# Kernel tuning notes

Hardware: AMD Instinct MI355X
Metric: run time of the kernel (lower is better)

## Reference

```python
import jax, jax.numpy as jnp
import numpy as np


def setup_inputs() -> dict:
    key = jax.random.key(0)
    k1, k2, k3 = jax.random.split(key, 3)
    B, H, S, D = 2, 16, 2048, 64
    return {
        "q": jax.random.normal(k1, (B, H, S, D), dtype=jnp.float32),
        "k": jax.random.normal(k2, (B, H, S, D), dtype=jnp.float32),
        "v": jax.random.normal(k3, (B, H, S, D), dtype=jnp.float32),
        "chunk_size": 256,
    }


def reference(q, k, v, chunk_size):
    # Chunked Based linear attention: linear (K^T V) + rank-3 quadratic (K x K x V)
    # inter-chunk state recurrence (shifted/exclusive cumsum over chunks) plus the
    # intra-chunk causal part with kernel  s = q.k;  phi = s + 0.5*s^2.
    B, H, S, D = q.shape
    C = chunk_size
    N = S // C
    scale = D ** (-0.5)

    qc = (q * scale).reshape(B, H, N, C, D)
    kc = k.reshape(B, H, N, C, D)
    vc = v.reshape(B, H, N, C, D)

    # ---- linear inter-chunk state: shifted cumsum of K^T V per chunk ----
    KV = jnp.einsum("bhncd,bhnce->bhnde", kc, vc)            # (B,H,N,D,D)
    S_lin = jnp.cumsum(KV, axis=2) - KV                       # exclusive cumsum
    o_lin = jnp.einsum("bhncd,bhnde->bhnce", qc, S_lin)

    # ---- quadratic inter-chunk state: shifted cumsum of sum_c K_d K_e V_f ----
    KKV = jnp.einsum("bhncd,bhnce,bhncf->bhndef", kc, kc, vc)  # (B,H,N,D,D,D)
    S_quad = jnp.cumsum(KKV, axis=2) - KKV                     # exclusive cumsum
    o_quad = 0.5 * jnp.einsum("bhndef,bhncd,bhnce->bhncf", S_quad, qc, qc)

    # ---- intra-chunk causal quadratic attention ----
    A = jnp.einsum("bhncd,bhnmd->bhncm", qc, kc)               # (B,H,N,C,C)
    mask = jnp.tril(jnp.ones((C, C), dtype=bool))
    Ak = jnp.where(mask, A + 0.5 * A * A, 0.0)
    o_intra = jnp.einsum("bhncm,bhnmf->bhncf", Ak, vc)

    out = (o_lin + o_quad + o_intra).reshape(B, H, S, D)
    return out
```

## Files before the change

kernel.cpp:

```cpp
#include <hip/hip_runtime.h>
#include <stdint.h>

#define SEQ  2048
#define DH   64
#define BH_N 32
#define SCALE 0.125f

typedef __attribute__((ext_vector_type(8))) short short8;
typedef __attribute__((ext_vector_type(4))) short short4b;
typedef __attribute__((ext_vector_type(4))) float f32x4;

static __device__ __forceinline__ unsigned short f2bf(float f) {
  unsigned int u = __float_as_uint(f);
  u += 0x7fffu + ((u >> 16) & 1u);
  return (unsigned short)(u >> 16);
}
#if __has_builtin(__builtin_amdgcn_cvt_pk_bf16_f32)
typedef __attribute__((ext_vector_type(2))) __bf16 bf16x2;
static __device__ __forceinline__ unsigned packbf(float a, float b) {
  return __builtin_bit_cast(unsigned, __builtin_amdgcn_cvt_pk_bf16_f32(a, b));
}
#else
static __device__ __forceinline__ unsigned packbf(float a, float b) {
  unsigned ua = __float_as_uint(a); ua += 0x7fffu + ((ua >> 16) & 1u);
  unsigned ub = __float_as_uint(b); ub += 0x7fffu + ((ub >> 16) & 1u);
  return __builtin_amdgcn_perm(ub, ua, 0x07060302);
}
#endif

__global__ __launch_bounds__(256) void prep_kernel(
    const float* __restrict__ kin, const float* __restrict__ vin,
    unsigned short* __restrict__ kb2, unsigned short* __restrict__ vt2)
{
  const int sb = blockIdx.x;
  const int bh = blockIdx.y;
  const int t  = threadIdx.x;
  __shared__ __align__(16) unsigned short lds[4096];
  const size_t base  = ((size_t)bh * SEQ + (size_t)sb * 64) * DH;
  const size_t obase = ((size_t)bh * 32 + sb) * 4096;

  #pragma unroll
  for (int i = 0; i < 4; ++i) {
    int idx = i * 256 + t, key = idx >> 4, F = (idx & 15) * 4;
    float4 f = *reinterpret_cast<const float4*>(kin + base + key * DH + F);
    int c = (F >> 5) * 4 + ((F >> 3) & 3), jh = (F >> 2) & 1;
    uint2 pk; pk.x = packbf(f.x, f.y); pk.y = packbf(f.z, f.w);
    *reinterpret_cast<uint2*>(lds + (c * 64 + key) * 8 + jh * 4) = pk;
  }
  __syncthreads();
  #pragma unroll
  for (int uu = 0; uu < 2; ++uu) {
    int u = uu * 256 + t;
    *reinterpret_cast<uint4*>(kb2 + obase + u * 8) =
        *reinterpret_cast<const uint4*>(lds + u * 8);
  }
  __syncthreads();
  #pragma unroll
  for (int i = 0; i < 4; ++i) {
    int idx = i * 256 + t, key = idx >> 4, F = (idx & 15) * 4;
    float4 f = *reinterpret_cast<const float4*>(vin + base + key * DH + F);
    int kgp = key >> 5, qd = (key >> 2) & 3, jj = ((key >> 4) & 1) * 4 + (key & 3);
    int u0 = kgp * 256 + (F >> 4) * 64 + qd * 16 + (F & 15);
    lds[(u0 + 0) * 8 + jj] = f2bf(f.x);
    lds[(u0 + 1) * 8 + jj] = f2bf(f.y);
    lds[(u0 + 2) * 8 + jj] = f2bf(f.z);
    lds[(u0 + 3) * 8 + jj] = f2bf(f.w);
  }
  __syncthreads();
  #pragma unroll
  for (int uu = 0; uu < 2; ++uu) {
    int u = uu * 256 + t;
    *reinterpret_cast<uint4*>(vt2 + obase + u * 8) =
        *reinterpret_cast<const uint4*>(lds + u * 8);
  }
}

__global__ __launch_bounds__(256, 2) void attn_kernel(
    const float* __restrict__ q,
    const unsigned short* __restrict__ kb2,
    const unsigned short* __restrict__ vt2,
    float* __restrict__ out)
{
  const int b0   = blockIdx.x;
  const int bh   = b0 & 31;
  const int g    = b0 >> 5;
  const int j    = (g < 8) ? g : 23 - g;
  const int last = 2 * j + 1;
  const int tid  = threadIdx.x;
  const int w    = tid >> 6;
  const int lane = tid & 63;
  const int low  = lane & 15;
  const int quad = lane >> 4;
  const int rh   = w & 1;

  const int mytile = (w < 2) ? (2 * j + 1) : (2 * j);
  const int r0     = mytile * 64 + rh * 32;

  __shared__ __align__(16) unsigned short buf[2][8192];

  const unsigned short* kb_h = kb2 + (size_t)bh * 32 * 4096;
  const unsigned short* v2_h = vt2 + (size_t)bh * 32 * 4096;

  short8 aq[2][2];
  #pragma unroll
  for (int h = 0; h < 2; ++h) {
    const float* qp =
        q + ((size_t)bh * SEQ + r0 + h * 16 + low) * DH + quad * 8;
    #pragma unroll
    for (int ks = 0; ks < 2; ++ks) {
      float4 f0 = *reinterpret_cast<const float4*>(qp + ks * 32);
      float4 f1 = *reinterpret_cast<const float4*>(qp + ks * 32 + 4);
      uint4 uv;
      uv.x = packbf(f0.x * SCALE, f0.y * SCALE);
      uv.y = packbf(f0.z * SCALE, f0.w * SCALE);
      uv.z = packbf(f1.x * SCALE, f1.y * SCALE);
      uv.w = packbf(f1.z * SCALE, f1.w * SCALE);
      aq[h][ks] = __builtin_bit_cast(short8, uv);
    }
  }

  f32x4 oacc[2][4];
  #pragma unroll
  for (int h = 0; h < 2; ++h)
    #pragma unroll
    for (int i = 0; i < 4; ++i) oacc[h][i] = (f32x4){0.f, 0.f, 0.f, 0.f};

  const unsigned short* gsrc = (w < 2) ? kb_h : v2_h;
  const int ghalf  = (w & 1) * 2048;
  const int ldsoff = (w >> 1) * 4096 + ghalf;
  uint4 g0, g1, g2, g3;

  #define GLOAD(T)                                                             \
    do {                                                                       \
      const unsigned short* gs_ = gsrc + (size_t)(T) * 4096 + ghalf;           \
      g0 = *reinterpret_cast<const uint4*>(gs_ + 0 * 512 + lane * 8);          \
      g1 = *reinterpret_cast<const uint4*>(gs_ + 1 * 512 + lane * 8);          \
      g2 = *reinterpret_cast<const uint4*>(gs_ + 2 * 512 + lane * 8);          \
      g3 = *reinterpret_cast<const uint4*>(gs_ + 3 * 512 + lane * 8);          \
    } while (0)

  #define DSWRITE(B)                                                           \
    do {                                                                       \
      unsigned short* ld_ = &buf[B][ldsoff] + lane * 8;                        \
      *reinterpret_cast<uint4*>(ld_ + 0 * 512) = g0;                           \
      *reinterpret_cast<uint4*>(ld_ + 1 * 512) = g1;                           \
      *reinterpret_cast<uint4*>(ld_ + 2 * 512) = g2;                           \
      *reinterpret_cast<uint4*>(ld_ + 3 * 512) = g3;                           \
    } while (0)

  GLOAD(0);
  DSWRITE(0);

  for (int t = 0; t <= last; ++t) {
    const int bb = t & 1;
    if (t < last) GLOAD(t + 1);
    asm volatile("s_waitcnt lgkmcnt(0)" ::: "memory");
    __builtin_amdgcn_s_barrier();
    asm volatile("" ::: "memory");

    if (t <= mytile) {
      const bool diag = (t == mytile);
      const unsigned short* kT = &buf[bb][0];
      const unsigned short* vT = &buf[bb][4096];

      #pragma unroll
      for (int ntp = 0; ntp < 2; ++ntp) {
        short8 vf[4];
        #pragma unroll
        for (int ft = 0; ft < 4; ++ft)
          vf[ft] = *reinterpret_cast<const short8*>(
              vT + ((ntp * 4 + ft) * 64 + quad * 16 + low) * 8);

        #pragma unroll
        for (int sub = 0; sub < 2; ++sub) {
          const int nt = ntp * 2 + sub;
          f32x4 s0 = (f32x4){0.f, 0.f, 0.f, 0.f};
          f32x4 s1 = (f32x4){0.f, 0.f, 0.f, 0.f};
          #pragma unroll
          for (int ks = 0; ks < 2; ++ks) {
            short8 kf = *reinterpret_cast<const short8*>(
                kT + ((ks * 4 + quad) * 64 + nt * 16 + low) * 8);
            s0 = __builtin_amdgcn_mfma_f32_16x16x32_bf16(kf, aq[0][ks], s0, 0, 0, 0);
            s1 = __builtin_amdgcn_mfma_f32_16x16x32_bf16(kf, aq[1][ks], s1, 0, 0, 0);
          }
          #pragma unroll
          for (int h = 0; h < 2; ++h) {
            f32x4 sv = h ? s1 : s0;
            float pv[4];
            #pragma unroll
            for (int r = 0; r < 4; ++r) {
              float x = sv[r];
              pv[r] = __builtin_fmaf(0.5f * x, x, x);
            }
            if (diag) {
              #pragma unroll
              for (int r = 0; r < 4; ++r)
                if ((nt * 16 + quad * 4 + r) > (rh * 32 + h * 16 + low)) pv[r] = 0.f;
            }
            uint2 du; du.x = packbf(pv[0], pv[1]); du.y = packbf(pv[2], pv[3]);
            short4b pf = __builtin_bit_cast(short4b, du);
            #pragma unroll
            for (int ft = 0; ft < 4; ++ft) {
              short4b va = sub
                  ? __builtin_shufflevector(vf[ft], vf[ft], 4, 5, 6, 7)
                  : __builtin_shufflevector(vf[ft], vf[ft], 0, 1, 2, 3);
              oacc[h][ft] = __builtin_amdgcn_mfma_f32_16x16x16bf16_1k(
                  va, pf, oacc[h][ft], 0, 0, 0);
            }
          }
        }
      }
    }

    if (t < last) DSWRITE(bb ^ 1);
  }

  #pragma unroll
  for (int h = 0; h < 2; ++h)
    #pragma unroll
    for (int ft = 0; ft < 4; ++ft)
      *reinterpret_cast<f32x4*>(
          out + ((size_t)bh * SEQ + r0 + h * 16 + low) * DH + ft * 16 + quad * 4) =
          oacc[h][ft];
}

extern "C" void kernel_launch(void* const* d_in, const int* in_sizes, int n_in,
                              void* d_out, int out_size, void* d_ws, size_t ws_size,
                              hipStream_t stream)
{
  const float* q = (const float*)d_in[0];
  const float* k = (const float*)d_in[1];
  const float* v = (const float*)d_in[2];
  float* out = (float*)d_out;

  unsigned short* kb2 = (unsigned short*)d_ws;
  unsigned short* vt2 = kb2 + (size_t)BH_N * SEQ * DH;

  prep_kernel<<<dim3(32, BH_N), 256, 0, stream>>>(k, v, kb2, vt2);
  attn_kernel<<<512, 256, 0, stream>>>(q, kb2, vt2, out);
}
```

Measured before the change: 129.5 us.

## Use two waves per block, each owning a full 64-row query tile

Cuts the attention block from four waves to two. Each wave now handles 64 query rows (four 16-row groups) instead of 32, so every K fragment read from LDS feeds four MFMAs instead of two. Each wave also loads a whole 4096-element K or V tile into eight registers before staging it in LDS. This reduces LDS traffic per MFMA but doubles the accumulator and Q registers per wave and halves the waves per block, which may hurt latency hiding.

```diff
diff --git a/kernel.cpp b/kernel.cpp
--- a/kernel.cpp
+++ b/kernel.cpp
@@ -16,7 +16,6 @@
   return (unsigned short)(u >> 16);
 }
 #if __has_builtin(__builtin_amdgcn_cvt_pk_bf16_f32)
-typedef __attribute__((ext_vector_type(2))) __bf16 bf16x2;
 static __device__ __forceinline__ unsigned packbf(float a, float b) {
   return __builtin_bit_cast(unsigned, __builtin_amdgcn_cvt_pk_bf16_f32(a, b));
 }
@@ -75,7 +74,7 @@
   }
 }
 
-__global__ __launch_bounds__(256, 2) void attn_kernel(
+__global__ __launch_bounds__(128) void attn_kernel(
     const float* __restrict__ q,
     const unsigned short* __restrict__ kb2,
     const unsigned short* __restrict__ vt2,
@@ -86,24 +85,22 @@
   const int g    = b0 >> 5;
   const int j    = (g < 8) ? g : 23 - g;
   const int last = 2 * j + 1;
-  const int tid  = threadIdx.x;
-  const int w    = tid >> 6;
-  const int lane = tid & 63;
+  const int w    = threadIdx.x >> 6;
+  const int lane = threadIdx.x & 63;
   const int low  = lane & 15;
   const int quad = lane >> 4;
-  const int rh   = w & 1;
-
-  const int mytile = (w < 2) ? (2 * j + 1) : (2 * j);
-  const int r0     = mytile * 64 + rh * 32;
+
+  const int mytile = w ? (2 * j) : (2 * j + 1);
+  const int r0     = mytile * 64;
 
   __shared__ __align__(16) unsigned short buf[2][8192];
 
   const unsigned short* kb_h = kb2 + (size_t)bh * 32 * 4096;
   const unsigned short* v2_h = vt2 + (size_t)bh * 32 * 4096;
 
-  short8 aq[2][2];
-  #pragma unroll
-  for (int h = 0; h < 2; ++h) {
+  short8 aq[4][2];
+  #pragma unroll
+  for (int h = 0; h < 4; ++h) {
     const float* qp =
         q + ((size_t)bh * SEQ + r0 + h * 16 + low) * DH + quad * 8;
     #pragma unroll
@@ -119,33 +116,29 @@
     }
   }
 
-  f32x4 oacc[2][4];
-  #pragma unroll
-  for (int h = 0; h < 2; ++h)
+  f32x4 oacc[4][4];
+  #pragma unroll
+  for (int h = 0; h < 4; ++h)
     #pragma unroll
     for (int i = 0; i < 4; ++i) oacc[h][i] = (f32x4){0.f, 0.f, 0.f, 0.f};
 
-  const unsigned short* gsrc = (w < 2) ? kb_h : v2_h;
-  const int ghalf  = (w & 1) * 2048;
-  const int ldsoff = (w >> 1) * 4096 + ghalf;
-  uint4 g0, g1, g2, g3;
+  const unsigned short* gsrc = w ? v2_h : kb_h;
+  uint4 gr[8];
 
   #define GLOAD(T)                                                             \
     do {                                                                       \
-      const unsigned short* gs_ = gsrc + (size_t)(T) * 4096 + ghalf;           \
-      g0 = *reinterpret_cast<const uint4*>(gs_ + 0 * 512 + lane * 8);          \
-      g1 = *reinterpret_cast<const uint4*>(gs_ + 1 * 512 + lane * 8);          \
-      g2 = *reinterpret_cast<const uint4*>(gs_ + 2 * 512 + lane * 8);          \
-      g3 = *reinterpret_cast<const uint4*>(gs_ + 3 * 512 + lane * 8);          \
+      const unsigned short* gs_ = gsrc + (size_t)(T) * 4096;                   \
+      _Pragma("unroll")                                                        \
+      for (int r_ = 0; r_ < 8; ++r_)                                           \
+        gr[r_] = *reinterpret_cast<const uint4*>(gs_ + r_ * 512 + lane * 8);   \
     } while (0)
 
   #define DSWRITE(B)                                                           \
     do {                                                                       \
-      unsigned short* ld_ = &buf[B][ldsoff] + lane * 8;                        \
-      *reinterpret_cast<uint4*>(ld_ + 0 * 512) = g0;                           \
-      *reinterpret_cast<uint4*>(ld_ + 1 * 512) = g1;                           \
-      *reinterpret_cast<uint4*>(ld_ + 2 * 512) = g2;                           \
-      *reinterpret_cast<uint4*>(ld_ + 3 * 512) = g3;                           \
+      unsigned short* ld_ = &buf[B][w * 4096] + lane * 8;                      \
+      _Pragma("unroll")                                                        \
+      for (int r_ = 0; r_ < 8; ++r_)                                           \
+        *reinterpret_cast<uint4*>(ld_ + r_ * 512) = gr[r_];                    \
     } while (0)
 
   GLOAD(0);
@@ -174,28 +167,34 @@
         #pragma unroll
         for (int sub = 0; sub < 2; ++sub) {
           const int nt = ntp * 2 + sub;
-          f32x4 s0 = (f32x4){0.f, 0.f, 0.f, 0.f};
-          f32x4 s1 = (f32x4){0.f, 0.f, 0.f, 0.f};
-          #pragma unroll
-          for (int ks = 0; ks < 2; ++ks) {
-            short8 kf = *reinterpret_cast<const short8*>(
+          short8 kf[2];
+          #pragma unroll
+          for (int ks = 0; ks < 2; ++ks)
+            kf[ks] = *reinterpret_cast<const short8*>(
                 kT + ((ks * 4 + quad) * 64 + nt * 16 + low) * 8);
-            s0 = __builtin_amdgcn_mfma_f32_16x16x32_bf16(kf, aq[0][ks], s0, 0, 0, 0);
-            s1 = __builtin_amdgcn_mfma_f32_16x16x32_bf16(kf, aq[1][ks], s1, 0, 0, 0);
-          }
-          #pragma unroll
-          for (int h = 0; h < 2; ++h) {
-            f32x4 sv = h ? s1 : s0;
+
+          f32x4 s[4];
+          #pragma unroll
+          for (int h = 0; h < 4; ++h) s[h] = (f32x4){0.f, 0.f, 0.f, 0.f};
+          #pragma unroll
+          for (int ks = 0; ks < 2; ++ks)
+            #pragma unroll
+            for (int h = 0; h < 4; ++h)
+              s[h] = __builtin_amdgcn_mfma_f32_16x16x32_bf16(
+                  kf[ks], aq[h][ks], s[h], 0, 0, 0);
+
+          #pragma unroll
+          for (int h = 0; h < 4; ++h) {
             float pv[4];
             #pragma unroll
             for (int r = 0; r < 4; ++r) {
-              float x = sv[r];
+              float x = s[h][r];
               pv[r] = __builtin_fmaf(0.5f * x, x, x);
             }
             if (diag) {
               #pragma unroll
               for (int r = 0; r < 4; ++r)
-                if ((nt * 16 + quad * 4 + r) > (rh * 32 + h * 16 + low)) pv[r] = 0.f;
+                if ((nt * 16 + quad * 4 + r) > (h * 16 + low)) pv[r] = 0.f;
             }
             uint2 du; du.x = packbf(pv[0], pv[1]); du.y = packbf(pv[2], pv[3]);
             short4b pf = __builtin_bit_cast(short4b, du);
@@ -216,7 +215,7 @@
   }
 
   #pragma unroll
-  for (int h = 0; h < 2; ++h)
+  for (int h = 0; h < 4; ++h)
     #pragma unroll
     for (int ft = 0; ft < 4; ++ft)
       *reinterpret_cast<f32x4*>(
@@ -237,5 +236,5 @@
   unsigned short* vt2 = kb2 + (size_t)BH_N * SEQ * DH;
 
   prep_kernel<<<dim3(32, BH_N), 256, 0, stream>>>(k, v, kb2, vt2);
-  attn_kernel<<<512, 256, 0, stream>>>(q, kb2, vt2, out);
-}
+  attn_kernel<<<512, 128, 0, stream>>>(q, kb2, vt2, out);
+}
```

Result: slower. 179.6 us (+38.8%).
